# Kernel optimization log

Hardware: AMD Instinct MI355X
Metric: run time of the kernel (lower is better)

The kernel has to match this reference:

```python
import jax, jax.numpy as jnp
import numpy as np

S, B, H = 2048, 32, 1024

def setup_inputs() -> dict:
    key = jax.random.key(0)
    ks = jax.random.split(key, 5)
    hidden = jax.random.normal(ks[0], (B, H), dtype=jnp.float32)
    encoder_outputs = jax.random.normal(ks[1], (S, B, H), dtype=jnp.float32)
    source_lengths = jax.random.randint(ks[2], (B,), 1, S + 1, dtype=jnp.int32)
    attn_w = jax.random.normal(ks[3], (H, 2 * H), dtype=jnp.float32) / np.sqrt(2 * H)
    attn_b = jnp.zeros((H,), dtype=jnp.float32)
    v = jax.random.uniform(ks[4], (H,), dtype=jnp.float32)
    return {"hidden": hidden, "encoder_outputs": encoder_outputs,
            "source_lengths": source_lengths, "attn_w": attn_w,
            "attn_b": attn_b, "v": v}

def reference(hidden, encoder_outputs, source_lengths, attn_w, attn_b, v):
    s, b, h = encoder_outputs.shape
    # Broadcast decoder hidden over source positions: (S,B,H)
    hid = jnp.broadcast_to(hidden[None, :, :], (s, b, h))
    cat = jnp.concatenate([hid, encoder_outputs], axis=2)          # (S,B,2H)
    energy = jnp.tanh(jnp.einsum('sbk,hk->sbh', cat, attn_w) + attn_b)  # (S,B,H)
    scores = jnp.einsum('sbh,h->bs', energy, v)                     # (B,S)
    mask = jnp.arange(s)[None, :] < source_lengths[:, None]         # (B,S)
    scores = jnp.where(mask, scores, jnp.float32(-1e10))
    attention_weights = jax.nn.softmax(scores, axis=1)              # (B,S)
    context = jnp.einsum('bs,sbh->bh', attention_weights, encoder_outputs)
    return context, attention_weights
```

## Files before the change

### kernel.cpp

```cpp
#include <hip/hip_runtime.h>

#define S_DIM 2048
#define B_DIM 32
#define H_DIM 1024
#define ROWS  (S_DIM * B_DIM)

typedef __attribute__((ext_vector_type(4))) float    f32x4;
typedef __attribute__((ext_vector_type(8))) _Float16 f16x8;
typedef __attribute__((ext_vector_type(2))) __fp16   h16x2;

__device__ __forceinline__ unsigned short f16_bits(float f) {
  union { _Float16 h; unsigned short u; } cv;
  cv.h = (_Float16)f;
  return cv.u;
}

__device__ __forceinline__ float fast_tanh(float x) {
  x = fminf(15.0f, fmaxf(-15.0f, x));
  float z = __expf(-2.0f * x);
  return (1.0f - z) * __builtin_amdgcn_rcpf(1.0f + z);
}

__device__ __forceinline__ void load_lds16(const void* g, void* l) {
  __builtin_amdgcn_global_load_lds(
      (const __attribute__((address_space(1))) unsigned int*)g,
      (__attribute__((address_space(3))) unsigned int*)l, 16, 0, 0);
}

__global__ void prep_kernel(const float* __restrict__ hidden,
                            const float* __restrict__ attn_w,
                            const float* __restrict__ attn_b,
                            float* __restrict__ hp,
                            unsigned short* __restrict__ Bp,
                            float* __restrict__ scores,
                            float* __restrict__ ctx) {
  int bid = blockIdx.x, tid = threadIdx.x;
  if (bid < 64) {
    int hl = tid >> 4;
    int kp = tid & 15;
    int h  = bid * 16 + hl;
    const f32x4* wrow = (const f32x4*)(attn_w + (size_t)h * (2 * H_DIM)) + kp * 16;
    f32x4 w[16];
#pragma unroll
    for (int j = 0; j < 16; ++j) w[j] = wrow[j];
    float bias = attn_b[h];
    for (int b = 0; b < B_DIM; ++b) {
      const f32x4* xrow = (const f32x4*)(hidden + (size_t)b * H_DIM) + kp * 16;
      float s = 0.f;
#pragma unroll
      for (int j = 0; j < 16; ++j) {
        f32x4 x = xrow[j];
        s = fmaf(w[j].x, x.x, s); s = fmaf(w[j].y, x.y, s);
        s = fmaf(w[j].z, x.z, s); s = fmaf(w[j].w, x.w, s);
      }
      s += __shfl_xor(s, 1); s += __shfl_xor(s, 2);
      s += __shfl_xor(s, 4); s += __shfl_xor(s, 8);
      if (kp == 0) hp[(size_t)b * H_DIM + h] = s + bias;
    }
  } else if (bid < 576) {
    int id = (bid - 64) * 256 + tid;
    int slot = id & 7;
    int n    = (id >> 3) & 127;
    int step = (id >> 10) & 15;
    int g    = id >> 14;
    int sub  = slot ^ (n & 7);
    int h    = g * 128 + n;
    const float* src = attn_w + (size_t)h * (2 * H_DIM) + H_DIM + step * 64 + sub * 8;
    f32x4 a = *(const f32x4*)src;
    f32x4 b = *(const f32x4*)(src + 4);
    ushort4 lo, hi;
    lo.x = f16_bits(a.x); lo.y = f16_bits(a.y); lo.z = f16_bits(a.z); lo.w = f16_bits(a.w);
    hi.x = f16_bits(b.x); hi.y = f16_bits(b.y); hi.z = f16_bits(b.z); hi.w = f16_bits(b.w);
    *(ushort4*)(Bp + (size_t)id * 8)     = lo;
    *(ushort4*)(Bp + (size_t)id * 8 + 4) = hi;
  } else if (bid < 640) {
    int idx = (bid - 576) * 256 + tid;
    *(f32x4*)(scores + (size_t)idx * 4) = (f32x4){0.f, 0.f, 0.f, 0.f};
  } else {
    int idx = (bid - 640) * 256 + tid;
    *(f32x4*)(ctx + (size_t)idx * 4) = (f32x4){0.f, 0.f, 0.f, 0.f};
  }
}

__global__ __launch_bounds__(256, 4)
void gemm_scores_kernel(const float* __restrict__ enc,
                        const unsigned short* __restrict__ Bp,
                        const float* __restrict__ hp,
                        const float* __restrict__ v,
                        float* __restrict__ scores) {
  __shared__ __align__(16) unsigned short As[1024 * 8];
  __shared__ __align__(16) unsigned short Bs[1024 * 8];
  const int tid  = threadIdx.x;
  const int lane = tid & 63;
  const int wid  = tid >> 6;
  const int wm   = wid >> 1;
  const int wn   = wid & 1;
  const int m16  = lane & 15;
  const int quad = lane >> 4;
  const int rx   = m16 & 7;
  const int bid  = blockIdx.x;
  const int xcd  = bid & 7;
  const int slot = bid >> 3;
  const int t    = xcd * 64 + (slot >> 3);
  const int g    = slot & 7;

  f32x4 acc[4][4];
#pragma unroll
  for (int i = 0; i < 4; ++i)
#pragma unroll
    for (int j = 0; j < 4; ++j) acc[i][j] = (f32x4){0.f, 0.f, 0.f, 0.f};

  const float* aBase = enc + (size_t)t * 128 * H_DIM;
  const unsigned short* bBase = Bp + (size_t)g * 16 * 8192;

  int aR[4], aSub[4];
#pragma unroll
  for (int c = 0; c < 4; ++c) {
    int q = c * 256 + tid;
    aR[c] = q >> 3;
    aSub[c] = (q & 7) ^ (aR[c] & 7);
  }

  for (int step = 0; step < 16; ++step) {
    const unsigned short* bS = bBase + (size_t)step * 8192;
#pragma unroll
    for (int c = 0; c < 4; ++c) {
      int q = c * 256 + tid;
      load_lds16(bS + (size_t)q * 8, Bs + q * 8);
    }
#pragma unroll
    for (int c = 0; c < 4; ++c) {
      int q = c * 256 + tid;
      const float* s = aBase + (size_t)aR[c] * H_DIM + step * 64 + aSub[c] * 8;
      f32x4 a = *(const f32x4*)s;
      f32x4 b = *(const f32x4*)(s + 4);
      union { f16x8 v8; h16x2 h2[4]; } pk;
      pk.h2[0] = __builtin_amdgcn_cvt_pkrtz(a.x, a.y);
      pk.h2[1] = __builtin_amdgcn_cvt_pkrtz(a.z, a.w);
      pk.h2[2] = __builtin_amdgcn_cvt_pkrtz(b.x, b.y);
      pk.h2[3] = __builtin_amdgcn_cvt_pkrtz(b.z, b.w);
      *(f16x8*)(As + q * 8) = pk.v8;
    }
    __syncthreads();

#pragma unroll
    for (int ko = 0; ko < 2; ++ko) {
      int sl = (ko * 4 + quad) ^ rx;
      f16x8 af[4], bfr[4];
#pragma unroll
      for (int f = 0; f < 4; ++f) {
        int r = wm * 64 + f * 16 + m16;
        af[f] = *(const f16x8*)&As[r * 64 + sl * 8];
      }
#pragma unroll
      for (int f = 0; f < 4; ++f) {
        int n = wn * 64 + f * 16 + m16;
        bfr[f] = *(const f16x8*)&Bs[n * 64 + sl * 8];
      }
#pragma unroll
      for (int mf = 0; mf < 4; ++mf)
#pragma unroll
        for (int nf = 0; nf < 4; ++nf)
          acc[mf][nf] = __builtin_amdgcn_mfma_f32_16x16x32_f16(
              af[mf], bfr[nf], acc[mf][nf], 0, 0, 0);
    }
    __syncthreads();
  }

  const int row0 = t * 128, n0 = g * 128;
#pragma unroll
  for (int mf = 0; mf < 4; ++mf) {
#pragma unroll
    for (int reg = 0; reg < 4; ++reg) {
      int row_g = row0 + wm * 64 + mf * 16 + quad * 4 + reg;
      int b     = row_g & 31;
      int s     = row_g >> 5;
      float psum = 0.f;
#pragma unroll
      for (int nf = 0; nf < 4; ++nf) {
        int col = n0 + wn * 64 + nf * 16 + m16;
        float e = acc[mf][nf][reg] + hp[b * H_DIM + col];
        e = fast_tanh(e);
        psum = fmaf(e, v[col], psum);
      }
      psum += __shfl_xor(psum, 1);
      psum += __shfl_xor(psum, 2);
      psum += __shfl_xor(psum, 4);
      psum += __shfl_xor(psum, 8);
      if (m16 == 0) atomicAdd(&scores[b * S_DIM + s], psum);
    }
  }
}

__global__ void softmax_kernel(const float* __restrict__ scores,
                               const int* __restrict__ lens,
                               float* __restrict__ wout) {
  int b = blockIdx.x, tid = threadIdx.x;
  int len = lens[b];
  float vals[8];
  float m = -3.0e38f;
#pragma unroll
  for (int i = 0; i < 8; ++i) {
    int s = i * 256 + tid;
    float x = scores[b * S_DIM + s];
    vals[i] = (s < len) ? x : -3.0e38f;
    m = fmaxf(m, vals[i]);
  }
#pragma unroll
  for (int off = 32; off > 0; off >>= 1) m = fmaxf(m, __shfl_xor(m, off));
  __shared__ float redm[4], reds[4];
  int wid = tid >> 6, lane = tid & 63;
  if (lane == 0) redm[wid] = m;
  __syncthreads();
  m = fmaxf(fmaxf(redm[0], redm[1]), fmaxf(redm[2], redm[3]));

  float e[8];
  float sum = 0.f;
#pragma unroll
  for (int i = 0; i < 8; ++i) {
    int s = i * 256 + tid;
    e[i] = (s < len) ? __expf(vals[i] - m) : 0.f;
    sum += e[i];
  }
#pragma unroll
  for (int off = 32; off > 0; off >>= 1) sum += __shfl_xor(sum, off);
  if (lane == 0) reds[wid] = sum;
  __syncthreads();
  sum = reds[0] + reds[1] + reds[2] + reds[3];
  float inv = 1.0f / sum;
#pragma unroll
  for (int i = 0; i < 8; ++i)
    wout[b * S_DIM + i * 256 + tid] = e[i] * inv;
}

__global__ void context_kernel(const float* __restrict__ enc,
                               const float* __restrict__ wts,
                               const int* __restrict__ lens,
                               float* __restrict__ ctx) {
  int sc = blockIdx.x;
  int b  = blockIdx.y;
  int len = lens[b];
  int s0 = sc * 128;
  if (s0 >= len) return;
  int cnt = min(128, len - s0);
  int tid = threadIdx.x;
  f32x4 acc = (f32x4){0.f, 0.f, 0.f, 0.f};
  const float* wrow = wts + (size_t)b * S_DIM + s0;
#pragma unroll 4
  for (int i = 0; i < cnt; ++i) {
    float w = wrow[i];
    f32x4 e = *(const f32x4*)(enc + ((size_t)(s0 + i) * B_DIM + b) * H_DIM + tid * 4);
    acc.x = fmaf(w, e.x, acc.x);
    acc.y = fmaf(w, e.y, acc.y);
    acc.z = fmaf(w, e.z, acc.z);
    acc.w = fmaf(w, e.w, acc.w);
  }
  float* dst = ctx + (size_t)b * H_DIM + tid * 4;
  atomicAdd(dst + 0, acc.x);
  atomicAdd(dst + 1, acc.y);
  atomicAdd(dst + 2, acc.z);
  atomicAdd(dst + 3, acc.w);
}

extern "C" void kernel_launch(void* const* d_in, const int* in_sizes, int n_in,
                              void* d_out, int out_size, void* d_ws, size_t ws_size,
                              hipStream_t stream) {
  const float* hidden = (const float*)d_in[0];
  const float* enc    = (const float*)d_in[1];
  const int*   lens   = (const int*)d_in[2];
  const float* attn_w = (const float*)d_in[3];
  const float* attn_b = (const float*)d_in[4];
  const float* v      = (const float*)d_in[5];

  float* out_ctx = (float*)d_out;
  float* out_w   = (float*)d_out + B_DIM * H_DIM;

  char* p = (char*)d_ws;
  float* scores = (float*)p;               p += (size_t)B_DIM * S_DIM * 4;
  float* hp     = (float*)p;               p += (size_t)B_DIM * H_DIM * 4;
  unsigned short* Bp = (unsigned short*)p;

  hipLaunchKernelGGL(prep_kernel, dim3(672), dim3(256), 0, stream,
                     hidden, attn_w, attn_b, hp, Bp, scores, out_ctx);
  hipLaunchKernelGGL(gemm_scores_kernel, dim3(4096), dim3(256), 0, stream,
                     enc, Bp, hp, v, scores);
  hipLaunchKernelGGL(softmax_kernel, dim3(B_DIM), dim3(256), 0, stream,
                     scores, lens, out_w);
  hipLaunchKernelGGL(context_kernel, dim3(16, B_DIM), dim3(256), 0, stream,
                     enc, out_w, lens, out_ctx);
}
```

Before: 602.6 us.

## Rewrite scores GEMM as 256x256 tiles with double-buffered LDS pipeline

The scores GEMM moves from 128x128 tiles with 256 threads to 256x256 tiles with 512 threads (8 waves), and the grid drops from 4096 to 1024 blocks. LDS is double-buffered: fp32 encoder rows are loaded two K-tiles ahead into registers through inline asm, converted to fp16 and written to the next buffer while MFMAs run on the current one. Explicit waitcnt, sched_barrier and setprio calls interleave the loads with the matrix math, and the B prep layout is reordered to match. Larger tiles cut how often A and B are re-read from global memory, at the cost of more registers, fewer resident blocks and hand-tuned scheduling.

```diff
diff --git a/kernel.cpp b/kernel.cpp
--- a/kernel.cpp
+++ b/kernel.cpp
@@ -26,6 +26,23 @@
       (const __attribute__((address_space(1))) unsigned int*)g,
       (__attribute__((address_space(3))) unsigned int*)l, 16, 0, 0);
 }
+
+__device__ __forceinline__ f32x4 gload16(const float* p) {
+  f32x4 r;
+  asm volatile("global_load_dwordx4 %0, %1, off" : "=v"(r) : "v"(p) : "memory");
+  return r;
+}
+
+#define PRIO1 __builtin_amdgcn_s_setprio(1)
+#define PRIO0 __builtin_amdgcn_s_setprio(0)
+#define SBAR  __builtin_amdgcn_sched_barrier(0)
+#define BAR   __builtin_amdgcn_s_barrier
+#define VMC8() do { asm volatile("s_waitcnt vmcnt(8)" ::: "memory"); \
+                    __builtin_amdgcn_sched_barrier(0); } while (0)
+#define VMC0() do { asm volatile("s_waitcnt vmcnt(0)" ::: "memory"); \
+                    __builtin_amdgcn_sched_barrier(0); } while (0)
+#define LGKM0() do { asm volatile("s_waitcnt lgkmcnt(0)" ::: "memory"); \
+                     __builtin_amdgcn_sched_barrier(0); } while (0)
 
 __global__ void prep_kernel(const float* __restrict__ hidden,
                             const float* __restrict__ attn_w,
@@ -58,14 +75,15 @@
       if (kp == 0) hp[(size_t)b * H_DIM + h] = s + bias;
     }
   } else if (bid < 576) {
-    int id = (bid - 64) * 256 + tid;
-    int slot = id & 7;
-    int n    = (id >> 3) & 127;
-    int step = (id >> 10) & 15;
-    int g    = id >> 14;
-    int sub  = slot ^ (n & 7);
-    int h    = g * 128 + n;
-    const float* src = attn_w + (size_t)h * (2 * H_DIM) + H_DIM + step * 64 + sub * 8;
+    int id   = (bid - 64) * 256 + tid;
+    int p    = id & 7;
+    int r    = (id >> 3) & 127;
+    int half = (id >> 10) & 1;
+    int kt   = (id >> 11) & 15;
+    int g    = id >> 15;
+    int sub  = p ^ (r & 7);
+    int n    = g * 256 + half * 128 + r;
+    const float* src = attn_w + (size_t)n * (2 * H_DIM) + H_DIM + kt * 64 + sub * 8;
     f32x4 a = *(const f32x4*)src;
     f32x4 b = *(const f32x4*)(src + 4);
     ushort4 lo, hi;
@@ -82,104 +100,187 @@
   }
 }
 
-__global__ __launch_bounds__(256, 4)
+__global__ __launch_bounds__(512, 2)
 void gemm_scores_kernel(const float* __restrict__ enc,
                         const unsigned short* __restrict__ Bp,
                         const float* __restrict__ hp,
                         const float* __restrict__ v,
                         float* __restrict__ scores) {
-  __shared__ __align__(16) unsigned short As[1024 * 8];
-  __shared__ __align__(16) unsigned short Bs[1024 * 8];
+  __shared__ __align__(16) unsigned short Asl[2][16384];
+  __shared__ __align__(16) unsigned short Bsl[2][16384];
+
   const int tid  = threadIdx.x;
   const int lane = tid & 63;
   const int wid  = tid >> 6;
-  const int wm   = wid >> 1;
-  const int wn   = wid & 1;
+  const int wm   = wid >> 2;
+  const int wn   = wid & 3;
   const int m16  = lane & 15;
   const int quad = lane >> 4;
-  const int rx   = m16 & 7;
+  const int swz  = m16 & 7;
+
   const int bid  = blockIdx.x;
   const int xcd  = bid & 7;
   const int slot = bid >> 3;
-  const int t    = xcd * 64 + (slot >> 3);
-  const int g    = slot & 7;
-
-  f32x4 acc[4][4];
-#pragma unroll
-  for (int i = 0; i < 4; ++i)
+  const int t    = xcd * 32 + (slot >> 2);
+  const int g    = slot & 3;
+
+  const int c0  = ((0 * 4 + quad) ^ swz) * 8;
+  const int c1  = ((1 * 4 + quad) ^ swz) * 8;
+  const int rdA = wm * 8192 + m16 * 64;
+  const int rdB = (wn >> 1) * 8192 + ((wn & 1) * 64 + m16) * 64;
+
+  const int r0 = tid >> 3;
+  const int s0 = (tid & 7) ^ (r0 & 7);
+  const int r1 = (512 + tid) >> 3;
+  const int s1 = ((512 + tid) & 7) ^ (r1 & 7);
+  const int aoff0 = r0 * H_DIM + s0 * 8;
+  const int aoff1 = r1 * H_DIM + s1 * 8;
+  const float* encT = enc + (size_t)t * 256 * H_DIM;
+  const unsigned short* BpG = Bp + (size_t)g * 262144;
+
+  f32x4 acc[8][4];
+#pragma unroll
+  for (int i = 0; i < 8; ++i)
 #pragma unroll
     for (int j = 0; j < 4; ++j) acc[i][j] = (f32x4){0.f, 0.f, 0.f, 0.f};
 
-  const float* aBase = enc + (size_t)t * 128 * H_DIM;
-  const unsigned short* bBase = Bp + (size_t)g * 16 * 8192;
-
-  int aR[4], aSub[4];
-#pragma unroll
-  for (int c = 0; c < 4; ++c) {
-    int q = c * 256 + tid;
-    aR[c] = q >> 3;
-    aSub[c] = (q & 7) ^ (aR[c] & 7);
-  }
-
-  for (int step = 0; step < 16; ++step) {
-    const unsigned short* bS = bBase + (size_t)step * 8192;
-#pragma unroll
-    for (int c = 0; c < 4; ++c) {
-      int q = c * 256 + tid;
-      load_lds16(bS + (size_t)q * 8, Bs + q * 8);
-    }
-#pragma unroll
-    for (int c = 0; c < 4; ++c) {
-      int q = c * 256 + tid;
-      const float* s = aBase + (size_t)aR[c] * H_DIM + step * 64 + aSub[c] * 8;
-      f32x4 a = *(const f32x4*)s;
-      f32x4 b = *(const f32x4*)(s + 4);
-      union { f16x8 v8; h16x2 h2[4]; } pk;
-      pk.h2[0] = __builtin_amdgcn_cvt_pkrtz(a.x, a.y);
-      pk.h2[1] = __builtin_amdgcn_cvt_pkrtz(a.z, a.w);
-      pk.h2[2] = __builtin_amdgcn_cvt_pkrtz(b.x, b.y);
-      pk.h2[3] = __builtin_amdgcn_cvt_pkrtz(b.z, b.w);
-      *(f16x8*)(As + q * 8) = pk.v8;
-    }
-    __syncthreads();
-
-#pragma unroll
-    for (int ko = 0; ko < 2; ++ko) {
-      int sl = (ko * 4 + quad) ^ rx;
-      f16x8 af[4], bfr[4];
-#pragma unroll
-      for (int f = 0; f < 4; ++f) {
-        int r = wm * 64 + f * 16 + m16;
-        af[f] = *(const f16x8*)&As[r * 64 + sl * 8];
-      }
-#pragma unroll
-      for (int f = 0; f < 4; ++f) {
-        int n = wn * 64 + f * 16 + m16;
-        bfr[f] = *(const f16x8*)&Bs[n * 64 + sl * 8];
-      }
-#pragma unroll
-      for (int mf = 0; mf < 4; ++mf)
-#pragma unroll
-        for (int nf = 0; nf < 4; ++nf)
-          acc[mf][nf] = __builtin_amdgcn_mfma_f32_16x16x32_f16(
-              af[mf], bfr[nf], acc[mf][nf], 0, 0, 0);
-    }
-    __syncthreads();
-  }
-
-  const int row0 = t * 128, n0 = g * 128;
-#pragma unroll
-  for (int mf = 0; mf < 4; ++mf) {
+  f16x8 af[4][2];
+  f16x8 bf[2][2];
+  f32x4 rh0[4], rh1[4];
+
+#define ISSUE_A(HH, KT, R)                                                     \
+  {                                                                            \
+    const float* s_ = encT + (size_t)(HH)*131072 + (KT)*64;                    \
+    R[0] = gload16(s_ + aoff0);                                                \
+    R[1] = gload16(s_ + aoff0 + 4);                                            \
+    R[2] = gload16(s_ + aoff1);                                                \
+    R[3] = gload16(s_ + aoff1 + 4);                                            \
+  }
+
+#define CVT_WRITE(HH, R, DST)                                                  \
+  {                                                                            \
+    union { f16x8 v8; h16x2 h2[4]; } pk;                                       \
+    pk.h2[0] = __builtin_amdgcn_cvt_pkrtz(R[0].x, R[0].y);                     \
+    pk.h2[1] = __builtin_amdgcn_cvt_pkrtz(R[0].z, R[0].w);                     \
+    pk.h2[2] = __builtin_amdgcn_cvt_pkrtz(R[1].x, R[1].y);                     \
+    pk.h2[3] = __builtin_amdgcn_cvt_pkrtz(R[1].z, R[1].w);                     \
+    *(f16x8*)((DST) + (HH)*8192 + tid * 8) = pk.v8;                            \
+    pk.h2[0] = __builtin_amdgcn_cvt_pkrtz(R[2].x, R[2].y);                     \
+    pk.h2[1] = __builtin_amdgcn_cvt_pkrtz(R[2].z, R[2].w);                     \
+    pk.h2[2] = __builtin_amdgcn_cvt_pkrtz(R[3].x, R[3].y);                     \
+    pk.h2[3] = __builtin_amdgcn_cvt_pkrtz(R[3].z, R[3].w);                     \
+    *(f16x8*)((DST) + (HH)*8192 + 4096 + tid * 8) = pk.v8;                     \
+  }
+
+#define STAGE_B(HH, KT, DST)                                                   \
+  {                                                                            \
+    const unsigned short* s_ = BpG + (KT)*16384 + (HH)*8192 + tid * 8;         \
+    load_lds16(s_, (DST) + (HH)*8192 + tid * 8);                               \
+    load_lds16(s_ + 4096, (DST) + (HH)*8192 + 4096 + tid * 8);                 \
+  }
+
+#define A_READ(MH, SRC)                                                        \
+  _Pragma("unroll")                                                            \
+  for (int f = 0; f < 4; ++f) {                                                \
+    af[f][0] = *(const f16x8*)((SRC) + rdA + ((MH)*64 + f * 16) * 64 + c0);    \
+    af[f][1] = *(const f16x8*)((SRC) + rdA + ((MH)*64 + f * 16) * 64 + c1);    \
+  }
+
+#define B_READ(NH, SRC)                                                        \
+  _Pragma("unroll")                                                            \
+  for (int f = 0; f < 2; ++f) {                                                \
+    bf[f][0] = *(const f16x8*)((SRC) + rdB + ((NH)*32 + f * 16) * 64 + c0);    \
+    bf[f][1] = *(const f16x8*)((SRC) + rdB + ((NH)*32 + f * 16) * 64 + c1);    \
+  }
+
+#define MFMA_Q(MH, NH)                                                         \
+  _Pragma("unroll")                                                            \
+  for (int mf = 0; mf < 4; ++mf) {                                             \
+    _Pragma("unroll")                                                          \
+    for (int nf = 0; nf < 2; ++nf) {                                           \
+      acc[(MH)*4 + mf][(NH)*2 + nf] = __builtin_amdgcn_mfma_f32_16x16x32_f16(  \
+          af[mf][0], bf[nf][0], acc[(MH)*4 + mf][(NH)*2 + nf], 0, 0, 0);       \
+      acc[(MH)*4 + mf][(NH)*2 + nf] = __builtin_amdgcn_mfma_f32_16x16x32_f16(  \
+          af[mf][1], bf[nf][1], acc[(MH)*4 + mf][(NH)*2 + nf], 0, 0, 0);       \
+    }                                                                          \
+  }
+
+  ISSUE_A(0, 0, rh0);
+  ISSUE_A(1, 0, rh1);
+  STAGE_B(0, 0, &Bsl[0][0]);
+  STAGE_B(1, 0, &Bsl[0][0]);
+  VMC8();
+  CVT_WRITE(0, rh0, &Asl[0][0]);
+  ISSUE_A(0, 1, rh0);
+  VMC8();
+  CVT_WRITE(1, rh1, &Asl[0][0]);
+  ISSUE_A(1, 1, rh1);
+  VMC8();
+  LGKM0();
+  BAR(); SBAR;
+
+#define TILE(CUR, T)                                                           \
+  {                                                                            \
+    unsigned short* Ac = &Asl[CUR][0];                                         \
+    unsigned short* Bc = &Bsl[CUR][0];                                         \
+    unsigned short* An = &Asl[(CUR) ^ 1][0];                                   \
+    unsigned short* Bn = &Bsl[(CUR) ^ 1][0];                                   \
+    const int ktB = ((T) + 1 < 16) ? (T) + 1 : 15;                             \
+    const int ktA = ((T) + 2 < 16) ? (T) + 2 : 15;                             \
+                                                           \
+    A_READ(0, Ac); B_READ(0, Bc);                                              \
+    STAGE_B(0, ktB, Bn);                                                       \
+    BAR(); LGKM0();                                                            \
+    PRIO1; MFMA_Q(0, 0); PRIO0;                                                \
+    BAR(); SBAR;                                                               \
+                                               \
+    B_READ(1, Bc);                                                             \
+    STAGE_B(1, ktB, Bn);                                                       \
+    BAR(); LGKM0();                                                            \
+    PRIO1; MFMA_Q(0, 1); PRIO0;                                                \
+    BAR(); SBAR;                                                               \
+             \
+    A_READ(1, Ac);                                                             \
+    VMC8();                                                                    \
+    CVT_WRITE(0, rh0, An);                                                     \
+    ISSUE_A(0, ktA, rh0);                                                      \
+    BAR(); LGKM0();                                                            \
+    PRIO1; MFMA_Q(1, 1); PRIO0;                                                \
+    BAR(); SBAR;                                                               \
+           \
+    B_READ(0, Bc);                                                             \
+    VMC8();                                                                    \
+    CVT_WRITE(1, rh1, An);                                                     \
+    ISSUE_A(1, ktA, rh1);                                                      \
+    BAR(); LGKM0();                                                            \
+    PRIO1; MFMA_Q(1, 0); PRIO0;                                                \
+    VMC8();                                                                    \
+    BAR(); SBAR;                                                               \
+  }
+
+#pragma unroll 1
+  for (int tt = 0; tt < 16; tt += 2) {
+    TILE(0, tt);
+    TILE(1, tt + 1);
+  }
+
+  VMC0();
+
+  const int row0 = t * 256 + wm * 128;
+  const int col0 = g * 256 + wn * 64;
+#pragma unroll
+  for (int a = 0; a < 8; ++a) {
+    const int rbase = row0 + (a >> 2) * 64 + (a & 3) * 16 + quad * 4;
 #pragma unroll
     for (int reg = 0; reg < 4; ++reg) {
-      int row_g = row0 + wm * 64 + mf * 16 + quad * 4 + reg;
-      int b     = row_g & 31;
-      int s     = row_g >> 5;
+      int row_g = rbase + reg;
+      int bb    = row_g & 31;
+      int ss    = row_g >> 5;
       float psum = 0.f;
 #pragma unroll
-      for (int nf = 0; nf < 4; ++nf) {
-        int col = n0 + wn * 64 + nf * 16 + m16;
-        float e = acc[mf][nf][reg] + hp[b * H_DIM + col];
+      for (int b2 = 0; b2 < 4; ++b2) {
+        int col = col0 + (b2 >> 1) * 32 + (b2 & 1) * 16 + m16;
+        float e = acc[a][b2][reg] + hp[bb * H_DIM + col];
         e = fast_tanh(e);
         psum = fmaf(e, v[col], psum);
       }
@@ -187,9 +288,16 @@
       psum += __shfl_xor(psum, 2);
       psum += __shfl_xor(psum, 4);
       psum += __shfl_xor(psum, 8);
-      if (m16 == 0) atomicAdd(&scores[b * S_DIM + s], psum);
+      if (m16 == 0) atomicAdd(&scores[bb * S_DIM + ss], psum);
     }
   }
+#undef TILE
+#undef MFMA_Q
+#undef B_READ
+#undef A_READ
+#undef STAGE_B
+#undef CVT_WRITE
+#undef ISSUE_A
 }
 
 __global__ void softmax_kernel(const float* __restrict__ scores,
@@ -282,7 +390,7 @@
 
   hipLaunchKernelGGL(prep_kernel, dim3(672), dim3(256), 0, stream,
                      hidden, attn_w, attn_b, hp, Bp, scores, out_ctx);
-  hipLaunchKernelGGL(gemm_scores_kernel, dim3(4096), dim3(256), 0, stream,
+  hipLaunchKernelGGL(gemm_scores_kernel, dim3(1024), dim3(512), 0, stream,
                      enc, Bp, hp, v, scores);
   hipLaunchKernelGGL(softmax_kernel, dim3(B_DIM), dim3(256), 0, stream,
                      scores, lens, out_w);
```

Result: slower. 628.3 us (+4.3%).
